# Kernel optimization log

Measured on AMD Instinct MI355X. Metric: run time of the kernel, lower is better.

Reference implementation:

```python
import jax, jax.numpy as jnp
import numpy as np

N_SAMPLES, N_TIME, N_FEAT = 64, 4, 64
N_ENTITIES = 10000
D = N_TIME * N_FEAT  # 256
K = 10


def setup_inputs() -> dict:
    key = jax.random.key(0)
    k1, k2 = jax.random.split(key)
    query = jax.random.uniform(k1, (N_SAMPLES, N_TIME, N_FEAT), dtype=jnp.float32)
    # module state: self.enity_info, flattened view must be [n_entities, D]
    enity_info = jax.random.uniform(k2, (N_ENTITIES, D), dtype=jnp.float32)
    return {"query": query, "enity_info": enity_info, "k": K}


def reference(query, enity_info, k):
    n_samples = query.shape[0]
    q = query.reshape(n_samples, -1)                 # [n, d]
    e = enity_info.reshape(enity_info.shape[0], -1)  # [m, d]
    # pairwise Jaccard: sum(min) / sum(max) over feature dim
    inter = jnp.sum(jnp.minimum(q[:, None, :], e[None, :, :]), axis=2)  # [n, m]
    union = jnp.sum(jnp.maximum(q[:, None, :], e[None, :, :]), axis=2)  # [n, m]
    jaccard = inter / union                                             # [n, m]
    # torch.topk largest=True, sorted=True -> lax.top_k (descending)
    _, top_idx = jax.lax.top_k(jaccard, k)
    # torch.topk largest=False, sorted=True -> ascending smallest: top_k of negated
    _, bot_idx = jax.lax.top_k(-jaccard, k)
    return top_idx, bot_idx
```

## Files before the change

### kernel.cpp

```cpp
#include <hip/hip_runtime.h>
#include <math.h>
#include <limits.h>

#define NQ     64
#define NE     10000
#define K      10
#define NSTRIP 250
#define EPB    40
#define TPB    1024
#define EPP    5
#define SLOT   11
#define SCALE  8388608.0f

__device__ __forceinline__ bool better_top(double v, int i, double v2, int i2) {
    return (v > v2) || (v == v2 && i < i2);
}
__device__ __forceinline__ bool better_bot(double v, int i, double v2, int i2) {
    return (v < v2) || (v == v2 && i < i2);
}

template <bool TOP>
__device__ __forceinline__ void merge_slots16(double* Mv, unsigned short* Mi, int A, int B) {
    double ov[K]; unsigned short oi[K];
    int a = 0, b = 0;
#pragma unroll
    for (int o = 0; o < K; ++o) {
        double va = Mv[A * SLOT + a]; int ia = Mi[A * SLOT + a];
        double vb = Mv[B * SLOT + b]; int ib = Mi[B * SLOT + b];
        bool pick = TOP ? better_top(va, ia, vb, ib) : better_bot(va, ia, vb, ib);
        ov[o] = pick ? va : vb;
        oi[o] = (unsigned short)(pick ? ia : ib);
        if (pick) ++a; else ++b;
    }
#pragma unroll
    for (int o = 0; o < K; ++o) { Mv[A * SLOT + o] = ov[o]; Mi[A * SLOT + o] = oi[o]; }
}

#define CSWAP(CMP, v, ii, A, B)                                            \
    {                                                                      \
        bool c_ = CMP(v[B], ii[B], v[A], ii[A]);                           \
        double tv_ = c_ ? v[B] : v[A]; double uv_ = c_ ? v[A] : v[B];      \
        int    ti_ = c_ ? ii[B] : ii[A]; int ui_ = c_ ? ii[A] : ii[B];     \
        v[A] = tv_; v[B] = uv_; ii[A] = ti_; ii[B] = ui_;                  \
    }
#define SORT5(CMP, v, ii)            \
    CSWAP(CMP, v, ii, 0, 1) CSWAP(CMP, v, ii, 3, 4) CSWAP(CMP, v, ii, 2, 4) \
    CSWAP(CMP, v, ii, 2, 3) CSWAP(CMP, v, ii, 0, 3) CSWAP(CMP, v, ii, 0, 2) \
    CSWAP(CMP, v, ii, 1, 4) CSWAP(CMP, v, ii, 1, 3) CSWAP(CMP, v, ii, 1, 2)

__global__ __launch_bounds__(256) void ent_sums(const float* __restrict__ E,
                                                unsigned* __restrict__ Se) {
    const int w = threadIdx.x >> 6, l = threadIdx.x & 63;
    const int j = blockIdx.x * 4 + w;
    float4 v = reinterpret_cast<const float4*>(E)[(size_t)j * 64 + l];
    unsigned s = (unsigned)(v.x * SCALE) + (unsigned)(v.y * SCALE)
               + (unsigned)(v.z * SCALE) + (unsigned)(v.w * SCALE);
#pragma unroll
    for (int m = 1; m < 64; m <<= 1) s += (unsigned)__shfl_xor((int)s, m, 64);
    if (l == 0) Se[j] = s;
}

__global__ __launch_bounds__(TPB, 3) void jac_part(
        const float* __restrict__ Q, const float* __restrict__ E,
        const unsigned* __restrict__ Se,
        double* __restrict__ pvT, double* __restrict__ pvB,
        int* __restrict__ piT, int* __restrict__ piB) {
    __shared__ uint4 QT[2][2048];
    __shared__ uint4 EB[16][65];

    const int t    = threadIdx.x;
    const int l    = t & 63;
    const int w    = t >> 6;
    const int q    = l >> 1;
    const int sub  = l & 1;
    const int half = w & 1;
    const int p    = w >> 1;
    const int strip = blockIdx.x;
    const int q64  = half * 32 + q;

    unsigned* SqP = (unsigned*)&EB[0][0];
    {
        const int sq = t >> 4, c = t & 15;
        unsigned acc = 0;
#pragma unroll
        for (int r = 0; r < 4; ++r) {
            const int gg = c + 16 * r;
            float4 v = reinterpret_cast<const float4*>(Q)[sq * 64 + gg];
            uint4 u;
            u.x = (unsigned)(v.x * SCALE); u.y = (unsigned)(v.y * SCALE);
            u.z = (unsigned)(v.z * SCALE); u.w = (unsigned)(v.w * SCALE);
            QT[sq >> 5][(gg & 31) * 64 + 2 * (sq & 31) + (gg >> 5)] = u;
            acc += u.x + u.y + u.z + u.w;
        }
        SqP[t] = acc;
    }
    __syncthreads();
    unsigned Sq = 0;
#pragma unroll
    for (int pp = 0; pp < 16; ++pp) Sq += SqP[q64 * 16 + ((pp + q64) & 15)];
    __syncthreads();

    const uint4* QTt = &QT[half][0];
    uint4* ebw = &EB[w][l + (l >> 5)];
    const uint4* ebr = &EB[w][sub * 33];

    const int jb = strip * EPB;
    unsigned recI[EPP], recU[EPP];
    const float4* E4 = (const float4*)E;

    float4 er = E4[(size_t)(jb + p) * 64 + l];
    unsigned se = Se[jb + p];

#pragma unroll
    for (int s = 0; s < EPP; ++s) {
        const int sn = (s + 1 < EPP) ? s + 1 : s;
        float4 ern = E4[(size_t)(jb + p + 8 * sn) * 64 + l];
        unsigned sen = Se[jb + p + 8 * sn];

        uint4 eu;
        eu.x = (unsigned)(er.x * SCALE); eu.y = (unsigned)(er.y * SCALE);
        eu.z = (unsigned)(er.z * SCALE); eu.w = (unsigned)(er.w * SCALE);
        *ebw = eu;

        unsigned a0 = 0, a1 = 0;
#pragma unroll 8
        for (int g = 0; g < 32; ++g) {
            uint4 qv = QTt[g * 64 + l];
            uint4 ev = ebr[g];
            a0 += min(qv.x, ev.x) + min(qv.y, ev.y);
            a1 += min(qv.z, ev.z) + min(qv.w, ev.w);
        }
        unsigned ih = a0 + a1;
        unsigned inter = ih + (unsigned)__shfl_xor((int)ih, 1, 64);
        recI[s] = inter;
        recU[s] = Sq + se - inter;
        er = ern; se = sen;
    }

    double jv[EPP]; int ji[EPP];
#pragma unroll
    for (int s = 0; s < EPP; ++s) {
        jv[s] = (double)recI[s] / (double)recU[s];
        ji[s] = jb + p + 8 * s;
    }
    double av[EPP]; int ai[EPP]; double bv[EPP]; int bi[EPP];
#pragma unroll
    for (int s = 0; s < EPP; ++s) { av[s] = jv[s]; ai[s] = ji[s]; bv[s] = jv[s]; bi[s] = ji[s]; }
    SORT5(better_top, av, ai)
    SORT5(better_bot, bv, bi)

    __syncthreads();
    double*         Mv = ((double*)&QT[0][0]) + half * (256 * SLOT);
    unsigned short* Mi = ((unsigned short*)&EB[0][0]) + half * (256 * SLOT);
    const int slot = p * 32 + q;

    if (sub == 0) {
#pragma unroll
        for (int o = 0; o < EPP; ++o) { Mv[slot * SLOT + o] = av[o]; Mi[slot * SLOT + o] = (unsigned short)ai[o]; }
#pragma unroll
        for (int o = EPP; o < K; ++o) { Mv[slot * SLOT + o] = -INFINITY; Mi[slot * SLOT + o] = 0xFFFFu; }
    }
    __syncthreads();
    for (int s = 4; s >= 1; s >>= 1) {
        if (sub == 0 && p < s) merge_slots16<true>(Mv, Mi, p * 32 + q, (p + s) * 32 + q);
        __syncthreads();
    }
    if (sub == 0 && p == 0) {
        const size_t off = ((size_t)q64 * NSTRIP + strip) * K;
#pragma unroll
        for (int o = 0; o < K; ++o) { pvT[off + o] = Mv[q * SLOT + o]; piT[off + o] = (int)Mi[q * SLOT + o]; }
    }
    __syncthreads();

    if (sub == 0) {
#pragma unroll
        for (int o = 0; o < EPP; ++o) { Mv[slot * SLOT + o] = bv[o]; Mi[slot * SLOT + o] = (unsigned short)bi[o]; }
#pragma unroll
        for (int o = EPP; o < K; ++o) { Mv[slot * SLOT + o] = INFINITY; Mi[slot * SLOT + o] = 0xFFFFu; }
    }
    __syncthreads();
    for (int s = 4; s >= 1; s >>= 1) {
        if (sub == 0 && p < s) merge_slots16<false>(Mv, Mi, p * 32 + q, (p + s) * 32 + q);
        __syncthreads();
    }
    if (sub == 0 && p == 0) {
        const size_t off = ((size_t)q64 * NSTRIP + strip) * K;
#pragma unroll
        for (int o = 0; o < K; ++o) { pvB[off + o] = Mv[q * SLOT + o]; piB[off + o] = (int)Mi[q * SLOT + o]; }
    }
}

__global__ __launch_bounds__(256) void final_extract(
        const double* __restrict__ pvT, const double* __restrict__ pvB,
        const int* __restrict__ piT, const int* __restrict__ piB,
        int* __restrict__ out) {
    __shared__ double Lv[NSTRIP * K];
    __shared__ int    Li[NSTRIP * K];
    __shared__ double Wv[4];
    __shared__ int    Wi[4], Wo[4];
    __shared__ int    res[K];

    const int b   = blockIdx.x;
    const int q   = b >> 1;
    const bool top = (b & 1) == 0;
    const int t   = threadIdx.x;
    const int l   = t & 63;
    const int w   = t >> 6;

    const double* V = (top ? pvT : pvB) + (size_t)q * NSTRIP * K;
    const int*    I = (top ? piT : piB) + (size_t)q * NSTRIP * K;

    for (int i = t; i < NSTRIP * K; i += 256) {
        double v = V[i];
        Lv[i] = top ? v : -v;
        Li[i] = I[i];
    }
    __syncthreads();

    int h = 0;
    double hv = (t < NSTRIP) ? Lv[t * K] : -INFINITY;
    int    hi = (t < NSTRIP) ? Li[t * K] : INT_MAX;

    for (int r = 0; r < K; ++r) {
        double v = hv; int idx = hi; int own = t;
#pragma unroll
        for (int m = 1; m < 64; m <<= 1) {
            double ov = __shfl_xor(v, m, 64);
            int    oi = __shfl_xor(idx, m, 64);
            int    oo = __shfl_xor(own, m, 64);
            if (better_top(ov, oi, v, idx)) { v = ov; idx = oi; own = oo; }
        }
        if (l == 0) { Wv[w] = v; Wi[w] = idx; Wo[w] = own; }
        __syncthreads();
        double gv = Wv[0]; int gi = Wi[0], go = Wo[0];
#pragma unroll
        for (int ww = 1; ww < 4; ++ww)
            if (better_top(Wv[ww], Wi[ww], gv, gi)) { gv = Wv[ww]; gi = Wi[ww]; go = Wo[ww]; }
        if (t == go) {
            ++h;
            bool ok = h < K;
            hv = ok ? Lv[t * K + h] : -INFINITY;
            hi = ok ? Li[t * K + h] : INT_MAX;
        }
        if (t == 0) res[r] = gi;
        __syncthreads();
    }

    if (t < K) out[(top ? 0 : NQ * K) + q * K + t] = res[t];
}

extern "C" void kernel_launch(void* const* d_in, const int* in_sizes, int n_in,
                              void* d_out, int out_size, void* d_ws, size_t ws_size,
                              hipStream_t stream) {
    const float* Q = (const float*)d_in[0];
    const float* E = (const float*)d_in[1];
    int* out = (int*)d_out;

    char* ws = (char*)d_ws;
    unsigned* Se  = (unsigned*)(ws);
    double*   pvT = (double*)(ws + 40960);
    double*   pvB = (double*)(ws + 1320960);
    int*      piT = (int*)   (ws + 2600960);
    int*      piB = (int*)   (ws + 3240960);

    hipLaunchKernelGGL(ent_sums, dim3(NE / 4), dim3(256), 0, stream, E, Se);
    hipLaunchKernelGGL(jac_part, dim3(NSTRIP), dim3(TPB), 0, stream,
                       Q, E, Se, pvT, pvB, piT, piB);
    hipLaunchKernelGGL(final_extract, dim3(NQ * 2), dim3(256), 0, stream,
                       pvT, pvB, piT, piB, out);
}
```

Before: 49.39 us.

## Stage all entity rows in shared memory and reuse each query load across them

Each wave now writes all five of its entity rows into a larger shared buffer up front. The inner loop then loads each query vector once and computes the min-sums against all five entities, instead of re-reading the query tile once per entity. This cuts LDS traffic for the query tile by about a factor of five. In exchange, shared memory use grows from about 16 KB to roughly 80 KB per block and register pressure rises, while the launch bound is raised to 4 blocks per CU, which may no longer fit in LDS or registers.

New measurement: 47.50 us. 3.8% less time.

```diff
diff --git a/kernel.cpp b/kernel.cpp
--- a/kernel.cpp
+++ b/kernel.cpp
@@ -60,13 +60,13 @@
     if (l == 0) Se[j] = s;
 }
 
-__global__ __launch_bounds__(TPB, 3) void jac_part(
+__global__ __launch_bounds__(TPB, 4) void jac_part(
         const float* __restrict__ Q, const float* __restrict__ E,
         const unsigned* __restrict__ Se,
         double* __restrict__ pvT, double* __restrict__ pvB,
         int* __restrict__ piT, int* __restrict__ piB) {
     __shared__ uint4 QT[2][2048];
-    __shared__ uint4 EB[16][65];
+    __shared__ uint4 EB[16][EPP][65];
 
     const int t    = threadIdx.x;
     const int l    = t & 63;
@@ -78,7 +78,7 @@
     const int strip = blockIdx.x;
     const int q64  = half * 32 + q;
 
-    unsigned* SqP = (unsigned*)&EB[0][0];
+    unsigned* SqP = (unsigned*)&EB[0][0][0];
     {
         const int sq = t >> 4, c = t & 15;
         unsigned acc = 0;
@@ -101,40 +101,44 @@
     __syncthreads();
 
     const uint4* QTt = &QT[half][0];
-    uint4* ebw = &EB[w][l + (l >> 5)];
-    const uint4* ebr = &EB[w][sub * 33];
-
     const int jb = strip * EPB;
-    unsigned recI[EPP], recU[EPP];
     const float4* E4 = (const float4*)E;
 
-    float4 er = E4[(size_t)(jb + p) * 64 + l];
-    unsigned se = Se[jb + p];
-
 #pragma unroll
     for (int s = 0; s < EPP; ++s) {
-        const int sn = (s + 1 < EPP) ? s + 1 : s;
-        float4 ern = E4[(size_t)(jb + p + 8 * sn) * 64 + l];
-        unsigned sen = Se[jb + p + 8 * sn];
-
+        float4 er = E4[(size_t)(jb + p + 8 * s) * 64 + l];
         uint4 eu;
         eu.x = (unsigned)(er.x * SCALE); eu.y = (unsigned)(er.y * SCALE);
         eu.z = (unsigned)(er.z * SCALE); eu.w = (unsigned)(er.w * SCALE);
-        *ebw = eu;
-
-        unsigned a0 = 0, a1 = 0;
-#pragma unroll 8
-        for (int g = 0; g < 32; ++g) {
-            uint4 qv = QTt[g * 64 + l];
-            uint4 ev = ebr[g];
-            a0 += min(qv.x, ev.x) + min(qv.y, ev.y);
-            a1 += min(qv.z, ev.z) + min(qv.w, ev.w);
-        }
-        unsigned ih = a0 + a1;
+        EB[w][s][l + (l >> 5)] = eu;
+    }
+    unsigned se[EPP];
+#pragma unroll
+    for (int s = 0; s < EPP; ++s) se[s] = Se[jb + p + 8 * s];
+
+    const uint4* ebr = &EB[w][0][sub * 33];
+    unsigned a0[EPP], a1[EPP];
+#pragma unroll
+    for (int s = 0; s < EPP; ++s) { a0[s] = 0; a1[s] = 0; }
+
+#pragma unroll 4
+    for (int g = 0; g < 32; ++g) {
+        uint4 qv = QTt[g * 64 + l];
+#pragma unroll
+        for (int s = 0; s < EPP; ++s) {
+            uint4 ev = ebr[s * 65 + g];
+            a0[s] += min(qv.x, ev.x) + min(qv.y, ev.y);
+            a1[s] += min(qv.z, ev.z) + min(qv.w, ev.w);
+        }
+    }
+
+    unsigned recI[EPP], recU[EPP];
+#pragma unroll
+    for (int s = 0; s < EPP; ++s) {
+        unsigned ih = a0[s] + a1[s];
         unsigned inter = ih + (unsigned)__shfl_xor((int)ih, 1, 64);
         recI[s] = inter;
-        recU[s] = Sq + se - inter;
-        er = ern; se = sen;
+        recU[s] = Sq + se[s] - inter;
     }
 
     double jv[EPP]; int ji[EPP];
@@ -151,7 +155,7 @@
 
     __syncthreads();
     double*         Mv = ((double*)&QT[0][0]) + half * (256 * SLOT);
-    unsigned short* Mi = ((unsigned short*)&EB[0][0]) + half * (256 * SLOT);
+    unsigned short* Mi = ((unsigned short*)&EB[0][0][0]) + half * (256 * SLOT);
     const int slot = p * 32 + q;
 
     if (sub == 0) {
```
